# Optimization experiments

Hardware: AMD Instinct MI355X
Metric: run time of the kernel (lower is better)

Reference implementation:

```python
import jax, jax.numpy as jnp
import numpy as np

EMBED_SIZE = 512
SCALE = EMBED_SIZE ** 0.5  # note: sqrt(embed_size), not sqrt(head_dim), per source


def setup_inputs() -> dict:
    key = jax.random.key(0)
    kq, kk, kv = jax.random.split(key, 3)
    B, H, S, D = 4, 8, 2048, 64
    query = jax.random.normal(kq, (B, H, S, D), dtype=jnp.float32)
    key_t = jax.random.normal(kk, (B, H, S, D), dtype=jnp.float32)
    value = jax.random.normal(kv, (B, S, H, D), dtype=jnp.float32)  # [b, kv_len, h, d]
    return {"query": query, "key": key_t, "value": value}


def reference(query, key, value):
    # scores: [b, h, q, k]
    scores = jnp.einsum('bhqf,bhkf->bhqk', query, key)
    weight = jax.nn.softmax(scores / SCALE, axis=3)
    # value is [b, l, h, d]; output [b, q, h, d]
    out = jnp.einsum('bhql,blhd->bqhd', weight, value)
    return out
```

## Files before the change

### kernel.cpp

```cpp
#include <hip/hip_runtime.h>
#include <stdint.h>

#define NB 4
#define NH 8
#define NS 2048
#define ND 64
#define BQ 128
#define TK 64
#define KP 72
#define NIT (NS/TK)

typedef __bf16  bf16x8 __attribute__((ext_vector_type(8)));
typedef float   f32x16 __attribute__((ext_vector_type(16)));

__device__ __forceinline__ uint32_t pkbf(float x, float y) {
  uint32_t ax = __builtin_bit_cast(uint32_t, x) + 0x8000u;
  uint32_t ay = __builtin_bit_cast(uint32_t, y) + 0x8000u;
  return __builtin_amdgcn_perm(ay, ax, 0x07060302u);
}
__device__ __forceinline__ unsigned short bfu(float x) {
  return (unsigned short)((__builtin_bit_cast(uint32_t, x) + 0x8000u) >> 16);
}

__global__ __launch_bounds__(256, 2) void fa_fwd(
    const float* __restrict__ Q, const float* __restrict__ K,
    const float* __restrict__ V, float* __restrict__ O)
{
  __shared__ __attribute__((aligned(16))) unsigned short Klds[TK*KP];
  __shared__ __attribute__((aligned(16))) unsigned short Vt [ND*KP];

  const int tid = threadIdx.x, wid = tid>>6, lane = tid&63;
  const int l31 = lane&31, h = lane>>5;
  const int bh = blockIdx.y, b = bh>>3, hh = bh&7;
  const int q0 = blockIdx.x * BQ;

  const float* Qb = Q + ((size_t)bh*NS + q0)*ND;
  const float* Kb = K + (size_t)bh*NS*ND;
  const float* Vb = V + ((size_t)b*NS*NH + hh)*ND;
  float*       Ob = O + ((size_t)b*NS*NH + hh)*ND;

  const float kSc = 1.44269504088896340736f / 22.6274169979695207808f;

  bf16x8 qf[4];
  {
    const float* qp = Qb + (size_t)(wid*32 + l31)*ND + 8*h;
#pragma unroll
    for (int k=0;k<4;++k){
      float4 a = *(const float4*)(qp + 16*k);
      float4 c = *(const float4*)(qp + 16*k + 4);
      uint4 u = make_uint4(pkbf(a.x*kSc,a.y*kSc), pkbf(a.z*kSc,a.w*kSc),
                           pkbf(c.x*kSc,c.y*kSc), pkbf(c.z*kSc,c.w*kSc));
      qf[k] = __builtin_bit_cast(bf16x8, u);
    }
  }

  const int krow0 = tid>>3, koct = tid&7;

  float4 kst[2][2], vst[4];
  auto load_tile = [&](int kb){
#pragma unroll
    for (int i=0;i<2;++i){
      const float* kp = Kb + (size_t)(kb + krow0 + 32*i)*ND + koct*8;
      kst[i][0] = *(const float4*)kp;
      kst[i][1] = *(const float4*)(kp+4);
    }
#pragma unroll
    for (int i=0;i<4;++i)
      vst[i] = *(const float4*)(Vb + (size_t)(kb + lane)*(NH*ND) + (wid+4*i)*4);
  };
  auto store_tile = [&](){
#pragma unroll
    for (int i=0;i<2;++i){
      uint4 w = make_uint4(pkbf(kst[i][0].x,kst[i][0].y), pkbf(kst[i][0].z,kst[i][0].w),
                           pkbf(kst[i][1].x,kst[i][1].y), pkbf(kst[i][1].z,kst[i][1].w));
      *(uint4*)&Klds[(size_t)(krow0+32*i)*KP + koct*8] = w;
    }
#pragma unroll
    for (int i=0;i<4;++i){
      int d0 = (wid+4*i)*4;
      Vt[(size_t)(d0+0)*KP + lane] = bfu(vst[i].x);
      Vt[(size_t)(d0+1)*KP + lane] = bfu(vst[i].y);
      Vt[(size_t)(d0+2)*KP + lane] = bfu(vst[i].z);
      Vt[(size_t)(d0+3)*KP + lane] = bfu(vst[i].w);
    }
  };

  load_tile(0);
  store_tile();
  __syncthreads();

  const f32x16 zero = {0,0,0,0,0,0,0,0,0,0,0,0,0,0,0,0};
  f32x16 acc[2] = {zero, zero};
  float lsum = 0.f;

  for (int kt=0; kt<NIT; ++kt){
    load_tile(((kt+1)&(NIT-1))*TK);

    f32x16 st[2];
#pragma unroll
    for (int t=0;t<2;++t){
      st[t] = zero;
#pragma unroll
      for (int k=0;k<4;++k){
        bf16x8 kf = *(const bf16x8*)&Klds[(size_t)(32*t+l31)*KP + 16*k + 8*h];
        st[t] = __builtin_amdgcn_mfma_f32_32x32x16_bf16(kf, qf[k], st[t], 0,0,0);
      }
    }

    uint32_t P0[2][4], P1[2][4];
#pragma unroll
    for (int t=0;t<2;++t)
#pragma unroll
      for (int u=0;u<4;++u){
        float p0 = __builtin_amdgcn_exp2f(st[t][4*u+0]);
        float p1 = __builtin_amdgcn_exp2f(st[t][4*u+1]);
        float p2 = __builtin_amdgcn_exp2f(st[t][4*u+2]);
        float p3 = __builtin_amdgcn_exp2f(st[t][4*u+3]);
        lsum += (p0+p1)+(p2+p3);
        P0[t][u] = pkbf(p0,p1);
        P1[t][u] = pkbf(p2,p3);
      }

    uint32_t X0[2][2], X1[2][2];
#pragma unroll
    for (int t=0;t<2;++t)
#pragma unroll
      for (int m=0;m<2;++m){
        uint32_t y0 = h ? P0[t][2*m] : P0[t][2*m+1];
        uint32_t y1 = h ? P1[t][2*m] : P1[t][2*m+1];
        X0[t][m] = (uint32_t)__shfl_xor((int)y0, 32, 64);
        X1[t][m] = (uint32_t)__shfl_xor((int)y1, 32, 64);
      }
    bf16x8 pf[4];
#pragma unroll
    for (int k=0;k<4;++k){
      int t = k>>1, m = k&1;
      uint32_t lo0 = h ? X0[t][m]     : P0[t][2*m];
      uint32_t lo1 = h ? X1[t][m]     : P1[t][2*m];
      uint32_t hi0 = h ? P0[t][2*m+1] : X0[t][m];
      uint32_t hi1 = h ? P1[t][2*m+1] : X1[t][m];
      uint4 u = make_uint4(lo0, lo1, hi0, hi1);
      pf[k] = __builtin_bit_cast(bf16x8, u);
    }

#pragma unroll
    for (int g=0;g<2;++g)
#pragma unroll
      for (int k=0;k<4;++k){
        bf16x8 vf = *(const bf16x8*)&Vt[(size_t)(32*g+l31)*KP + 16*k + 8*h];
        acc[g] = __builtin_amdgcn_mfma_f32_32x32x16_bf16(vf, pf[k], acc[g], 0,0,0);
      }

    __syncthreads();
    store_tile();
    __syncthreads();
  }

  lsum += __shfl_xor(lsum, 32, 64);
  const float inv = 1.0f / lsum;
  const int q = q0 + wid*32 + l31;
  float* op = Ob + (size_t)q*(NH*ND);
#pragma unroll
  for (int g=0; g<2; ++g)
#pragma unroll
    for (int u=0; u<4; ++u){
      float4 o;
      o.x = acc[g][4*u+0]*inv;
      o.y = acc[g][4*u+1]*inv;
      o.z = acc[g][4*u+2]*inv;
      o.w = acc[g][4*u+3]*inv;
      *(float4*)(op + 32*g + 8*u + 4*h) = o;
    }
}

extern "C" void kernel_launch(void* const* d_in, const int* in_sizes, int n_in,
                              void* d_out, int out_size, void* d_ws, size_t ws_size,
                              hipStream_t stream) {
  const float* Q = (const float*)d_in[0];
  const float* K = (const float*)d_in[1];
  const float* V = (const float*)d_in[2];
  float* O = (float*)d_out;
  dim3 grid(NS / BQ, NB * NH);
  hipLaunchKernelGGL(fa_fwd, grid, dim3(256), 0, stream, Q, K, V, O);
}
```

Before: 140.5 us.

## Software-pipeline QK^T and softmax-PV across iterations with triple-buffered LDS

Turns the K/V LDS tiles into a three-deep ring buffer and skews the loop, so the QK^T MFMAs for tile kt are issued next to the softmax and PV MFMAs for tile kt-1. Each iteration now needs one barrier instead of two, and the global loads are issued two tiles ahead. The row sum is split into four independent accumulators to shorten the add dependency chain. The cost is three times the LDS footprint and more live registers (the carried score tiles), which could lower occupancy below the requested 2 blocks per CU.

Measured after the change: 236.5 us. 68.3% more time.

```diff
diff --git a/kernel.cpp b/kernel.cpp
--- a/kernel.cpp
+++ b/kernel.cpp
@@ -12,6 +12,7 @@
 
 typedef __bf16  bf16x8 __attribute__((ext_vector_type(8)));
 typedef float   f32x16 __attribute__((ext_vector_type(16)));
+typedef float   f32x4  __attribute__((ext_vector_type(4)));
 
 __device__ __forceinline__ uint32_t pkbf(float x, float y) {
   uint32_t ax = __builtin_bit_cast(uint32_t, x) + 0x8000u;
@@ -26,8 +27,8 @@
     const float* __restrict__ Q, const float* __restrict__ K,
     const float* __restrict__ V, float* __restrict__ O)
 {
-  __shared__ __attribute__((aligned(16))) unsigned short Klds[TK*KP];
-  __shared__ __attribute__((aligned(16))) unsigned short Vt [ND*KP];
+  __shared__ __attribute__((aligned(16))) unsigned short Kl[3][TK*KP];
+  __shared__ __attribute__((aligned(16))) unsigned short Vt[3][ND*KP];
 
   const int tid = threadIdx.x, wid = tid>>6, lane = tid&63;
   const int l31 = lane&31, h = lane>>5;
@@ -55,7 +56,6 @@
   }
 
   const int krow0 = tid>>3, koct = tid&7;
-
   float4 kst[2][2], vst[4];
   auto load_tile = [&](int kb){
 #pragma unroll
@@ -68,59 +68,42 @@
     for (int i=0;i<4;++i)
       vst[i] = *(const float4*)(Vb + (size_t)(kb + lane)*(NH*ND) + (wid+4*i)*4);
   };
-  auto store_tile = [&](){
+  auto store_tile = [&](int bu){
 #pragma unroll
     for (int i=0;i<2;++i){
       uint4 w = make_uint4(pkbf(kst[i][0].x,kst[i][0].y), pkbf(kst[i][0].z,kst[i][0].w),
                            pkbf(kst[i][1].x,kst[i][1].y), pkbf(kst[i][1].z,kst[i][1].w));
-      *(uint4*)&Klds[(size_t)(krow0+32*i)*KP + koct*8] = w;
+      *(uint4*)&Kl[bu][(size_t)(krow0+32*i)*KP + koct*8] = w;
     }
 #pragma unroll
     for (int i=0;i<4;++i){
       int d0 = (wid+4*i)*4;
-      Vt[(size_t)(d0+0)*KP + lane] = bfu(vst[i].x);
-      Vt[(size_t)(d0+1)*KP + lane] = bfu(vst[i].y);
-      Vt[(size_t)(d0+2)*KP + lane] = bfu(vst[i].z);
-      Vt[(size_t)(d0+3)*KP + lane] = bfu(vst[i].w);
+      Vt[bu][(size_t)(d0+0)*KP + lane] = bfu(vst[i].x);
+      Vt[bu][(size_t)(d0+1)*KP + lane] = bfu(vst[i].y);
+      Vt[bu][(size_t)(d0+2)*KP + lane] = bfu(vst[i].z);
+      Vt[bu][(size_t)(d0+3)*KP + lane] = bfu(vst[i].w);
     }
   };
 
-  load_tile(0);
-  store_tile();
-  __syncthreads();
-
   const f32x16 zero = {0,0,0,0,0,0,0,0,0,0,0,0,0,0,0,0};
   f32x16 acc[2] = {zero, zero};
-  float lsum = 0.f;
+  f32x4  l4 = {0.f,0.f,0.f,0.f};
+  f32x16 stp[2];
 
-  for (int kt=0; kt<NIT; ++kt){
-    load_tile(((kt+1)&(NIT-1))*TK);
-
-    f32x16 st[2];
-#pragma unroll
-    for (int t=0;t<2;++t){
-      st[t] = zero;
-#pragma unroll
-      for (int k=0;k<4;++k){
-        bf16x8 kf = *(const bf16x8*)&Klds[(size_t)(32*t+l31)*KP + 16*k + 8*h];
-        st[t] = __builtin_amdgcn_mfma_f32_32x32x16_bf16(kf, qf[k], st[t], 0,0,0);
-      }
-    }
-
+  auto softmax_pv = [&](int pb){
     uint32_t P0[2][4], P1[2][4];
 #pragma unroll
     for (int t=0;t<2;++t)
 #pragma unroll
       for (int u=0;u<4;++u){
-        float p0 = __builtin_amdgcn_exp2f(st[t][4*u+0]);
-        float p1 = __builtin_amdgcn_exp2f(st[t][4*u+1]);
-        float p2 = __builtin_amdgcn_exp2f(st[t][4*u+2]);
-        float p3 = __builtin_amdgcn_exp2f(st[t][4*u+3]);
-        lsum += (p0+p1)+(p2+p3);
+        float p0 = __builtin_amdgcn_exp2f(stp[t][4*u+0]);
+        float p1 = __builtin_amdgcn_exp2f(stp[t][4*u+1]);
+        float p2 = __builtin_amdgcn_exp2f(stp[t][4*u+2]);
+        float p3 = __builtin_amdgcn_exp2f(stp[t][4*u+3]);
+        l4[0]+=p0; l4[1]+=p1; l4[2]+=p2; l4[3]+=p3;
         P0[t][u] = pkbf(p0,p1);
         P1[t][u] = pkbf(p2,p3);
       }
-
     uint32_t X0[2][2], X1[2][2];
 #pragma unroll
     for (int t=0;t<2;++t)
@@ -142,20 +125,49 @@
       uint4 u = make_uint4(lo0, lo1, hi0, hi1);
       pf[k] = __builtin_bit_cast(bf16x8, u);
     }
-
 #pragma unroll
     for (int g=0;g<2;++g)
 #pragma unroll
       for (int k=0;k<4;++k){
-        bf16x8 vf = *(const bf16x8*)&Vt[(size_t)(32*g+l31)*KP + 16*k + 8*h];
+        bf16x8 vf = *(const bf16x8*)&Vt[pb][(size_t)(32*g+l31)*KP + 16*k + 8*h];
         acc[g] = __builtin_amdgcn_mfma_f32_32x32x16_bf16(vf, pf[k], acc[g], 0,0,0);
       }
+  };
 
+  load_tile(0);
+  store_tile(0);
+  load_tile(TK);
+  __syncthreads();
+
+  for (int kt=0; kt<NIT; ++kt){
+    const int cb = kt % 3;
+    const int nb = (kt+1) % 3;
+    const int pb = (kt+2) % 3;
+
+    f32x16 st[2];
+#pragma unroll
+    for (int t=0;t<2;++t){
+      st[t] = zero;
+#pragma unroll
+      for (int k=0;k<4;++k){
+        bf16x8 kf = *(const bf16x8*)&Kl[cb][(size_t)(32*t+l31)*KP + 16*k + 8*h];
+        st[t] = __builtin_amdgcn_mfma_f32_32x32x16_bf16(kf, qf[k], st[t], 0,0,0);
+      }
+    }
+
+    if (kt) softmax_pv(pb);
+
+    store_tile(nb);
     __syncthreads();
-    store_tile();
-    __syncthreads();
+
+    load_tile(((kt+2)&(NIT-1))*TK);
+
+    stp[0] = st[0]; stp[1] = st[1];
   }
 
+  softmax_pv((NIT-1)%3);
+
+  float lsum = (l4[0]+l4[1]) + (l4[2]+l4[3]);
   lsum += __shfl_xor(lsum, 32, 64);
   const float inv = 1.0f / lsum;
   const int q = q0 + wid*32 + l31;
```
